# Kernel tuning notes

Hardware: AMD Instinct MI355X
Metric: run time of the kernel (lower is better)

## Reference

```python
import jax, jax.numpy as jnp
import numpy as np

D = 1024      # model dim
H = 16        # heads
DH = D // H   # head dim
T = 1024      # input tokens
B = 2         # batch
P = 4         # persistent tokens
WIN = 256     # sliding window
MH = 4 * D    # neural-memory hidden dim
FF = 4 * D    # ffn hidden dim
EPS = 1e-5


def _layernorm(x, g, b):
    m = jnp.mean(x, axis=-1, keepdims=True)
    v = jnp.mean((x - m) ** 2, axis=-1, keepdims=True)
    return (x - m) * jax.lax.rsqrt(v + EPS) * g + b


def setup_inputs() -> dict:
    key = jax.random.key(0)
    ks = jax.random.split(key, 12)
    s = 0.02
    return {
        "x": jax.random.normal(ks[0], (B, T, D), dtype=jnp.float32),
        "pmem": jax.random.normal(ks[1], (P, D), dtype=jnp.float32) * s,
        # neural memory MLP: dim -> MH -> dim (torch Linear convention W:(out,in))
        "mW1": jax.random.normal(ks[2], (MH, D), dtype=jnp.float32) * s,
        "mb1": jnp.zeros((MH,), dtype=jnp.float32),
        "mW2": jax.random.normal(ks[3], (D, MH), dtype=jnp.float32) * s,
        "mb2": jnp.zeros((D,), dtype=jnp.float32),
        "ln1_g": jnp.ones((D,), dtype=jnp.float32),
        "ln1_b": jnp.zeros((D,), dtype=jnp.float32),
        # MHA packed qkv in-proj and out-proj
        "Wqkv": jax.random.normal(ks[4], (3 * D, D), dtype=jnp.float32) * s,
        "bqkv": jnp.zeros((3 * D,), dtype=jnp.float32),
        "Wo": jax.random.normal(ks[5], (D, D), dtype=jnp.float32) * s,
        "bo": jnp.zeros((D,), dtype=jnp.float32),
        "ln2_g": jnp.ones((D,), dtype=jnp.float32),
        "ln2_b": jnp.zeros((D,), dtype=jnp.float32),
        "fW1": jax.random.normal(ks[6], (FF, D), dtype=jnp.float32) * s,
        "fb1": jnp.zeros((FF,), dtype=jnp.float32),
        "fW2": jax.random.normal(ks[7], (D, FF), dtype=jnp.float32) * s,
        "fb2": jnp.zeros((D,), dtype=jnp.float32),
    }


def _forward(x, pmem, mW1, mb1, mW2, mb2, ln1_g, ln1_b, Wqkv, bqkv, Wo, bo,
             ln2_g, ln2_b, fW1, fb1, fW2, fb2):
    Bc, Tc, Dc = x.shape
    # 1. retrieve from neural long-term memory: 2-layer MLP on x
    mem_ctx = jax.nn.relu(jnp.einsum('btd,hd->bth', x, mW1) + mb1)
    mem_ctx = jnp.einsum('bth,dh->btd', mem_ctx, mW2) + mb2
    # 2. concat persistent tokens, retrieved memory, x along sequence
    pers = jnp.broadcast_to(pmem[None], (Bc, P, Dc))
    aug = jnp.concatenate([pers, mem_ctx, x], axis=1)      # (B, L, D)
    L = aug.shape[1]
    # 3. sliding-window causal attention on norm1(aug)
    h = _layernorm(aug, ln1_g, ln1_b)
    qkv = jnp.einsum('bld,ed->ble', h, Wqkv) + bqkv        # (B, L, 3D)
    q, k, v = jnp.split(qkv, 3, axis=-1)
    q = q.reshape(Bc, L, H, DH)
    k = k.reshape(Bc, L, H, DH)
    v = v.reshape(Bc, L, H, DH)
    scale = 1.0 / np.sqrt(DH).astype(np.float32)
    scores = jnp.einsum('bqhd,bkhd->bhqk', q, k) * scale   # (B, H, L, L)
    i = jnp.arange(L)[:, None]
    j = jnp.arange(L)[None, :]
    allowed = (j <= i) & (j > i - WIN)                     # causal sliding window
    scores = jnp.where(allowed[None, None], scores, jnp.float32(-1e30))
    attn = jax.nn.softmax(scores, axis=-1)
    ctx = jnp.einsum('bhqk,bkhd->bqhd', attn, v).reshape(Bc, L, D)
    h_attn = jnp.einsum('bld,ed->ble', ctx, Wo) + bo
    # 4. residual + FFN
    h_res = aug + h_attn
    f = _layernorm(h_res, ln2_g, ln2_b)
    f = jax.nn.gelu(jnp.einsum('bld,fd->blf', f, fW1) + fb1, approximate=False)
    f = jnp.einsum('blf,df->bld', f, fW2) + fb2
    return h_res + f                                       # (B, P+2T, D)


def reference(x, pmem, mW1, mb1, mW2, mb2, ln1_g, ln1_b, Wqkv, bqkv, Wo, bo,
              ln2_g, ln2_b, fW1, fb1, fW2, fb2):
    return _forward(x, pmem, mW1, mb1, mW2, mb2, ln1_g, ln1_b, Wqkv, bqkv,
                    Wo, bo, ln2_g, ln2_b, fW1, fb1, fW2, fb2)
```

## Files before the change

kernel.cpp:

```cpp
#include <hip/hip_runtime.h>
#include <math.h>

#define D_   1024
#define H_   16
#define DH_  64
#define T_   1024
#define B_   2
#define P_   4
#define L_   2052
#define WIN_ 256
#define MH_  4096
#define FF_  4096

typedef __attribute__((ext_vector_type(8))) short bf16x8;
typedef __attribute__((ext_vector_type(4))) float f32x4;
typedef __attribute__((ext_vector_type(8))) unsigned short ush8;

__device__ __forceinline__ unsigned short f2bf(float f) {
  unsigned int u = __builtin_bit_cast(unsigned int, f);
  u += 0x7fffu + ((u >> 16) & 1u);
  return (unsigned short)(u >> 16);
}
__device__ __forceinline__ float bf2f(unsigned short h) {
  unsigned int u = ((unsigned int)h) << 16;
  return __builtin_bit_cast(float, u);
}

__device__ __forceinline__ void gl16(const unsigned short* g, unsigned short* l) {
  __builtin_amdgcn_global_load_lds(
      (const __attribute__((address_space(1))) unsigned int*)g,
      (__attribute__((address_space(3))) unsigned int*)l, 16, 0, 0);
}

__global__ __launch_bounds__(256)
void cvt7_k(const float* s0, unsigned short* d0, int n0,
            const float* s1, unsigned short* d1, int n1,
            const float* s2, unsigned short* d2, int n2,
            const float* s3, unsigned short* d3, int n3,
            const float* s4, unsigned short* d4, int n4,
            const float* s5, unsigned short* d5, int n5,
            const float* s6, unsigned short* d6, int n6) {
  const float* s; unsigned short* d; int n;
  switch (blockIdx.y) {
    case 0: s = s0; d = d0; n = n0; break;
    case 1: s = s1; d = d1; n = n1; break;
    case 2: s = s2; d = d2; n = n2; break;
    case 3: s = s3; d = d3; n = n3; break;
    case 4: s = s4; d = d4; n = n4; break;
    case 5: s = s5; d = d5; n = n5; break;
    default: s = s6; d = d6; n = n6; break;
  }
  int e = (blockIdx.x * 256 + threadIdx.x) * 4;
  if (e >= n) return;
  float4 v = *(const float4*)(s + e);
  ushort4 o;
  o.x = f2bf(v.x); o.y = f2bf(v.y); o.z = f2bf(v.z); o.w = f2bf(v.w);
  *(ushort4*)(d + e) = o;
}

__global__ __launch_bounds__(256)
void concat_ln1_k(const float* __restrict__ x, const float* __restrict__ pmem,
                  const float* __restrict__ p0, const float* __restrict__ p1,
                  const float* __restrict__ mb2, const float* __restrict__ g,
                  const float* __restrict__ bb,
                  float* __restrict__ aug, unsigned short* __restrict__ hln) {
  const int row = blockIdx.x;
  const int rl  = row % L_;
  const int b   = row / L_;
  const int tid = threadIdx.x;
  const int c   = tid * 4;
  float4 v;
  if (rl < P_) {
    v = *(const float4*)(pmem + rl * D_ + c);
  } else if (rl < P_ + T_) {
    size_t idx = (size_t)(b * T_ + (rl - P_)) * D_ + c;
    float4 a0 = *(const float4*)(p0 + idx);
    float4 a1 = *(const float4*)(p1 + idx);
    float4 bbv = *(const float4*)(mb2 + c);
    v = make_float4(a0.x + a1.x + bbv.x, a0.y + a1.y + bbv.y,
                    a0.z + a1.z + bbv.z, a0.w + a1.w + bbv.w);
  } else {
    v = *(const float4*)(x + (size_t)(b * T_ + (rl - P_ - T_)) * D_ + c);
  }
  *(float4*)(aug + (size_t)row * D_ + c) = v;
  float s  = v.x + v.y + v.z + v.w;
  float sq = v.x * v.x + v.y * v.y + v.z * v.z + v.w * v.w;
  #pragma unroll
  for (int o = 1; o < 64; o <<= 1) { s += __shfl_xor(s, o); sq += __shfl_xor(sq, o); }
  __shared__ float red[8];
  const int wid = tid >> 6;
  if ((tid & 63) == 0) { red[wid] = s; red[4 + wid] = sq; }
  __syncthreads();
  s  = red[0] + red[1] + red[2] + red[3];
  sq = red[4] + red[5] + red[6] + red[7];
  const float mean = s * (1.0f / D_);
  const float var  = sq * (1.0f / D_) - mean * mean;
  const float inv  = rsqrtf(var + 1e-5f);
  float4 gv = *(const float4*)(g + c);
  float4 bv = *(const float4*)(bb + c);
  unsigned short* dst = hln + (size_t)row * D_ + c;
  dst[0] = f2bf((v.x - mean) * inv * gv.x + bv.x);
  dst[1] = f2bf((v.y - mean) * inv * gv.y + bv.y);
  dst[2] = f2bf((v.z - mean) * inv * gv.z + bv.z);
  dst[3] = f2bf((v.w - mean) * inv * gv.w + bv.w);
}

__global__ void reduce10_k(const float* __restrict__ p0, const float* __restrict__ p1,
                           const float* __restrict__ hres, const float* __restrict__ fb2,
                           float* __restrict__ out) {
  int i = blockIdx.x * blockDim.x + threadIdx.x;
  if (i >= (B_ * L_ * D_) / 4) return;
  int e = i * 4;
  int d = e % D_;
  float4 a0 = *(const float4*)(p0 + e);
  float4 a1 = *(const float4*)(p1 + e);
  float4 hr = *(const float4*)(hres + e);
  float4 bb = *(const float4*)(fb2 + d);
  float4 v = make_float4(a0.x + a1.x + hr.x + bb.x, a0.y + a1.y + hr.y + bb.y,
                         a0.z + a1.z + hr.z + bb.z, a0.w + a1.w + hr.w + bb.w);
  *(float4*)(out + e) = v;
}

__global__ __launch_bounds__(256)
void layernorm_k(const float* __restrict__ in, const float* __restrict__ g,
                 const float* __restrict__ bb, unsigned short* __restrict__ out) {
  const int row = blockIdx.x;
  const int tid = threadIdx.x;
  const float* xr = in + (size_t)row * D_;
  float4 v = *(const float4*)(xr + tid * 4);
  float s  = v.x + v.y + v.z + v.w;
  float sq = v.x * v.x + v.y * v.y + v.z * v.z + v.w * v.w;
  #pragma unroll
  for (int o = 1; o < 64; o <<= 1) { s += __shfl_xor(s, o); sq += __shfl_xor(sq, o); }
  __shared__ float red[8];
  const int wid = tid >> 6;
  if ((tid & 63) == 0) { red[wid] = s; red[4 + wid] = sq; }
  __syncthreads();
  s  = red[0] + red[1] + red[2] + red[3];
  sq = red[4] + red[5] + red[6] + red[7];
  const float mean = s * (1.0f / D_);
  const float var  = sq * (1.0f / D_) - mean * mean;
  const float inv  = rsqrtf(var + 1e-5f);
  const int c = tid * 4;
  float4 gv = *(const float4*)(g + c);
  float4 bv = *(const float4*)(bb + c);
  unsigned short* dst = out + (size_t)row * D_ + c;
  dst[0] = f2bf((v.x - mean) * inv * gv.x + bv.x);
  dst[1] = f2bf((v.y - mean) * inv * gv.y + bv.y);
  dst[2] = f2bf((v.z - mean) * inv * gv.z + bv.z);
  dst[3] = f2bf((v.w - mean) * inv * gv.w + bv.w);
}

template<int ACT, int OUTBF, int RESID, int WM, int WN, int NWR, int NWC, int KS, int PART, int SWZ>
__global__ __launch_bounds__(KS * NWR * NWC * 64)
void gemm_bt_k(const unsigned short* __restrict__ A,
               const unsigned short* __restrict__ W,
               const float* __restrict__ bias,
               const float* __restrict__ resid,
               void* __restrict__ Cv,
               int M, int N, int K, int ldK, long long zstride) {
  constexpr int NW = NWR * NWC;
  constexpr int BM = NWR * WM * 16;
  constexpr int BN = NWC * WN * 16;
  constexpr int LPS = BM / (NW * 16) + BN / (NW * 16);
  constexpr int STG = 2 * KS * (BM + BN) * 32 * 2;
  constexpr int RED = (KS > 1) ? BM * BN * 4 : 0;
  constexpr int SBYTES = STG > RED ? STG : RED;
  __shared__ __align__(16) char smem[SBYTES];
  unsigned short* sA = (unsigned short*)smem;
  unsigned short* sB = sA + 2 * KS * BM * 32;

  const int tid  = threadIdx.x;
  const int lane = tid & 63;
  const int wv   = tid >> 6;
  const int grp  = wv / NW;
  const int wg   = wv % NW;
  const int wr   = wg / NWC, wc = wg % NWC;

  int lx = blockIdx.x, ly = blockIdx.y, lz = blockIdx.z;
  if (SWZ) {
    const unsigned int gX = gridDim.x, gY = gridDim.y, gZ = gridDim.z;
    const unsigned int nwg = gX * gY * gZ;
    const unsigned int flat = (blockIdx.z * gY + blockIdx.y) * gX + blockIdx.x;
    const unsigned int q = nwg >> 3;
    const unsigned int g = (flat & 7) * q + (flat >> 3);
    const unsigned int NC = gX * gZ;
    ly = g / NC;
    const unsigned int c = g % NC;
    lx = c / gZ;
    lz = c % gZ;
  }
  const int gm0 = ly * BM;
  const int gn0 = lx * BN;

  const int KperG = K / KS;
  const int NT    = KperG / 32;
  const int zofs  = PART ? lz * K : 0;

  const f32x4 fz = {0.f, 0.f, 0.f, 0.f};
  f32x4 acc[WM][WN];
  #pragma unroll
  for (int i = 0; i < WM; ++i)
    #pragma unroll
    for (int j = 0; j < WN; ++j) acc[i][j] = fz;

  const int srow = lane >> 2;
  const int skq  = (lane & 3) ^ ((lane >> 3) & 3);
  const int skc  = skq * 8;
  const unsigned short* gA = A + (size_t)(gm0 + srow) * ldK + grp * KperG + zofs + skc;
  const unsigned short* gB = W + (size_t)(gn0 + srow) * ldK + grp * KperG + zofs + skc;

  const int fr   = lane & 15;
  const int fkq  = lane >> 4;
  const int fofs = (fr * 4 + (fkq ^ ((fr >> 1) & 3))) * 8;

  auto stage = [&](int d, int k0) {
    unsigned short* dA = sA + (d * KS + grp) * BM * 32;
    unsigned short* dB = sB + (d * KS + grp) * BN * 32;
    #pragma unroll
    for (int t = 0; t < BM / (NW * 16); ++t) {
      const int rr = wg * 16 + t * NW * 16;
      gl16(gA + (size_t)rr * ldK + k0, dA + rr * 32);
    }
    #pragma unroll
    for (int t = 0; t < BN / (NW * 16); ++t) {
      const int rr = wg * 16 + t * NW * 16;
      gl16(gB + (size_t)rr * ldK + k0, dB + rr * 32);
    }
  };

  auto wait_lps = [&]() {
    if constexpr (LPS == 2)      asm volatile("s_waitcnt vmcnt(2)" ::: "memory");
    else if constexpr (LPS == 3) asm volatile("s_waitcnt vmcnt(3)" ::: "memory");
    else if constexpr (LPS == 4) asm volatile("s_waitcnt vmcnt(4)" ::: "memory");
    else                         asm volatile("s_waitcnt vmcnt(0)" ::: "memory");
  };

  stage(0, 0);
  stage(1, 32);
  wait_lps();
  __builtin_amdgcn_s_barrier();
  asm volatile("" ::: "memory");

  for (int kt = 0; kt < NT; ++kt) {
    const int d = kt & 1;
    const unsigned short* lA = sA + (d * KS + grp) * BM * 32;
    const unsigned short* lB = sB + (d * KS + grp) * BN * 32;
    bf16x8 af[WM], bfr[WN];
    #pragma unroll
    for (int i = 0; i < WM; ++i) af[i]  = *(const bf16x8*)&lA[(wr * WM + i) * 512 + fofs];
    #pragma unroll
    for (int j = 0; j < WN; ++j) bfr[j] = *(const bf16x8*)&lB[(wc * WN + j) * 512 + fofs];
    asm volatile("s_waitcnt lgkmcnt(0)" ::: "memory");
    __builtin_amdgcn_s_barrier();
    asm volatile("" ::: "memory");
    if (kt + 2 < NT) stage(d, (kt + 2) * 32);
    __builtin_amdgcn_s_setprio(1);
    #pragma unroll
    for (int i = 0; i < WM; ++i)
      #pragma unroll
      for (int j = 0; j < WN; ++j)
        acc[i][j] = __builtin_amdgcn_mfma_f32_16x16x32_bf16(af[i], bfr[j], acc[i][j], 0, 0, 0);
    __builtin_amdgcn_s_setprio(0);
    if (kt + 1 < NT) {
      if (kt + 2 < NT) wait_lps();
      else asm volatile("s_waitcnt vmcnt(0)" ::: "memory");
      __builtin_amdgcn_s_barrier();
      asm volatile("" ::: "memory");
    }
  }

  if (KS > 1) {
    __syncthreads();
    f32x4* sR = (f32x4*)smem;
    const int tg = tid & (NW * 64 - 1);
    for (int g = 1; g < KS; ++g) {
      if (grp == g) {
        #pragma unroll
        for (int i = 0; i < WM; ++i)
          #pragma unroll
          for (int j = 0; j < WN; ++j) sR[(tg * WM + i) * WN + j] = acc[i][j];
      }
      __syncthreads();
      if (grp == 0) {
        #pragma unroll
        for (int i = 0; i < WM; ++i)
          #pragma unroll
          for (int j = 0; j < WN; ++j) {
            f32x4 t = sR[(tg * WM + i) * WN + j];
            #pragma unroll
            for (int r = 0; r < 4; ++r) acc[i][j][r] += t[r];
          }
      }
      __syncthreads();
    }
    if (grp != 0) return;
  }

  const int rq = (lane >> 4) * 4;
  if (PART) {
    float* Pout = (float*)Cv + (size_t)lz * zstride;
    #pragma unroll
    for (int i = 0; i < WM; ++i) {
      #pragma unroll
      for (int j = 0; j < WN; ++j) {
        const int col = gn0 + wc * WN * 16 + j * 16 + fr;
        #pragma unroll
        for (int r = 0; r < 4; ++r) {
          const int row = gm0 + wr * WM * 16 + i * 16 + rq + r;
          if (row < M) Pout[(size_t)row * N + col] = acc[i][j][r];
        }
      }
    }
    return;
  }
  #pragma unroll
  for (int i = 0; i < WM; ++i) {
    #pragma unroll
    for (int j = 0; j < WN; ++j) {
      const int col = gn0 + wc * WN * 16 + j * 16 + fr;
      const float bcol = bias[col];
      #pragma unroll
      for (int r = 0; r < 4; ++r) {
        const int row = gm0 + wr * WM * 16 + i * 16 + rq + r;
        if (row < M) {
          float v = acc[i][j][r] + bcol;
          if (RESID) v += resid[(size_t)row * N + col];
          if (ACT == 1) v = fmaxf(v, 0.f);
          if (ACT == 2) {
            float t = 0.7978845608f * v * (1.0f + 0.044715f * v * v);
            float e = __expf(2.0f * t);
            v = v - __fdividef(v, e + 1.0f);
          }
          if (OUTBF) ((unsigned short*)Cv)[(size_t)row * N + col] = f2bf(v);
          else       ((float*)Cv)[(size_t)row * N + col] = v;
        }
      }
    }
  }
}

__global__ __launch_bounds__(256)
void attn_k(const unsigned short* __restrict__ qkv, unsigned short* __restrict__ ctx) {
  __shared__ unsigned short Kb[64][72];
  __shared__ unsigned short Vt[64][72];
  __shared__ unsigned short Ps[4][16][72];
  const int tid  = threadIdx.x;
  const int lane = tid & 63;
  const int w    = tid >> 6;
  const int l15  = lane & 15;
  const int l4   = lane >> 4;
  const int qb   = blockIdx.x * 64;
  const int h    = blockIdx.y;
  const int b    = blockIdx.z;

  int qrow = qb + w * 16 + l15;
  if (qrow >= L_) qrow = L_ - 1;
  const unsigned short* qp = qkv + ((size_t)(b * L_ + qrow)) * 3072 + h * 64;
  bf16x8 aq0, aq1;
  #pragma unroll
  for (int e = 0; e < 8; ++e) {
    aq0[e] = (short)f2bf(bf2f(qp[l4 * 8 + e]) * 0.125f);
    aq1[e] = (short)f2bf(bf2f(qp[32 + l4 * 8 + e]) * 0.125f);
  }

  const f32x4 fz = {0.f, 0.f, 0.f, 0.f};
  f32x4 acc_o[4];
  #pragma unroll
  for (int j = 0; j < 4; ++j) acc_o[j] = fz;
  float m_[4], ls[4];
  #pragma unroll
  for (int r = 0; r < 4; ++r) { m_[r] = -3.0e38f; ls[r] = 0.f; }

  int k0 = qb - WIN_;
  if (k0 < 0) k0 = 0;

  for (int kb = k0; kb <= qb; kb += 64) {
    #pragma unroll
    for (int c = tid; c < 512; c += 256) {
      const int row = c >> 3;
      const int cc  = (c & 7) * 8;
      const int g   = kb + row;
      ush8 kv8 = {0, 0, 0, 0, 0, 0, 0, 0}, vv8 = kv8;
      if (g < L_) {
        const unsigned short* base = qkv + ((size_t)(b * L_ + g)) * 3072 + h * 64 + cc;
        kv8 = *(const ush8*)(base + 1024);
        vv8 = *(const ush8*)(base + 2048);
      }
      *(ush8*)&Kb[row][cc] = kv8;
      #pragma unroll
      for (int e = 0; e < 8; ++e) Vt[cc + e][row] = vv8[e];
    }
    __syncthreads();

    f32x4 s[4];
    #pragma unroll
    for (int kt = 0; kt < 4; ++kt) {
      bf16x8 bk0 = *(const bf16x8*)&Kb[kt * 16 + l15][l4 * 8];
      bf16x8 bk1 = *(const bf16x8*)&Kb[kt * 16 + l15][32 + l4 * 8];
      f32x4 t = __builtin_amdgcn_mfma_f32_16x16x32_bf16(aq0, bk0, fz, 0, 0, 0);
      s[kt]   = __builtin_amdgcn_mfma_f32_16x16x32_bf16(aq1, bk1, t,  0, 0, 0);
    }

    #pragma unroll
    for (int r = 0; r < 4; ++r) {
      const int qg = qb + w * 16 + l4 * 4 + r;
      float rm = -3.0e38f;
      #pragma unroll
      for (int kt = 0; kt < 4; ++kt) {
        const int kg = kb + kt * 16 + l15;
        const bool ok = (kg <= qg) && (kg + WIN_ > qg);
        rm = fmaxf(rm, ok ? s[kt][r] : -3.0e38f);
      }
      rm = fmaxf(rm, __shfl_xor(rm, 1));
      rm = fmaxf(rm, __shfl_xor(rm, 2));
      rm = fmaxf(rm, __shfl_xor(rm, 4));
      rm = fmaxf(rm, __shfl_xor(rm, 8));
      const float mn = fmaxf(m_[r], rm);
      const float sf = __expf(m_[r] - mn);
      m_[r] = mn;
      float ps = 0.f;
      #pragma unroll
      for (int kt = 0; kt < 4; ++kt) {
        const int kg = kb + kt * 16 + l15;
        const bool ok = (kg <= qg) && (kg + WIN_ > qg);
        const float p = ok ? __expf(s[kt][r] - mn) : 0.f;
        ps += p;
        Ps[w][l4 * 4 + r][kt * 16 + l15] = f2bf(p);
      }
      ps += __shfl_xor(ps, 1);
      ps += __shfl_xor(ps, 2);
      ps += __shfl_xor(ps, 4);
      ps += __shfl_xor(ps, 8);
      ls[r] = ls[r] * sf + ps;
      #pragma unroll
      for (int j = 0; j < 4; ++j) acc_o[j][r] *= sf;
    }

    #pragma unroll
    for (int ks = 0; ks < 2; ++ks) {
      bf16x8 pa = *(const bf16x8*)&Ps[w][l15][ks * 32 + l4 * 8];
      #pragma unroll
      for (int j = 0; j < 4; ++j) {
        bf16x8 vb = *(const bf16x8*)&Vt[j * 16 + l15][ks * 32 + l4 * 8];
        acc_o[j] = __builtin_amdgcn_mfma_f32_16x16x32_bf16(pa, vb, acc_o[j], 0, 0, 0);
      }
    }
    __syncthreads();
  }

  #pragma unroll
  for (int r = 0; r < 4; ++r) {
    const int qg = qb + w * 16 + l4 * 4 + r;
    if (qg < L_) {
      const float inv = 1.0f / ls[r];
      unsigned short* dst = ctx + ((size_t)(b * L_ + qg)) * 1024 + h * 64 + l15;
      #pragma unroll
      for (int j = 0; j < 4; ++j) dst[j * 16] = f2bf(acc_o[j][r] * inv);
    }
  }
}

extern "C" void kernel_launch(void* const* d_in, const int* in_sizes, int n_in,
                              void* d_out, int out_size, void* d_ws, size_t ws_size,
                              hipStream_t stream) {
  (void)in_sizes; (void)n_in; (void)out_size; (void)ws_size;
  const float* x    = (const float*)d_in[0];
  const float* pmem = (const float*)d_in[1];
  const float* mW1  = (const float*)d_in[2];
  const float* mb1  = (const float*)d_in[3];
  const float* mW2  = (const float*)d_in[4];
  const float* mb2  = (const float*)d_in[5];
  const float* ln1g = (const float*)d_in[6];
  const float* ln1b = (const float*)d_in[7];
  const float* Wqkv = (const float*)d_in[8];
  const float* bqkv = (const float*)d_in[9];
  const float* Wo   = (const float*)d_in[10];
  const float* bo   = (const float*)d_in[11];
  const float* ln2g = (const float*)d_in[12];
  const float* ln2b = (const float*)d_in[13];
  const float* fW1  = (const float*)d_in[14];
  const float* fb1  = (const float*)d_in[15];
  const float* fW2  = (const float*)d_in[16];
  const float* fb2  = (const float*)d_in[17];
  float* outp = (float*)d_out;
  char* ws = (char*)d_ws;

  unsigned short* w1b   = (unsigned short*)(ws + 0ull);
  unsigned short* w2b   = (unsigned short*)(ws + 8388608ull);
  unsigned short* wqkvb = (unsigned short*)(ws + 16777216ull);
  unsigned short* wob   = (unsigned short*)(ws + 23068672ull);
  unsigned short* fw1b  = (unsigned short*)(ws + 25165824ull);
  unsigned short* fw2b  = (unsigned short*)(ws + 33554432ull);
  const size_t S = 41943040ull;
  float* aug  = (float*)(ws + S);
  float* hres = (float*)(ws + S + 16809984ull);
  unsigned short* hlnbuf = (unsigned short*)(ws + S + 33619968ull);
  char* R = ws + S + 42270720ull;
  unsigned short* xb   = (unsigned short*)(R);
  unsigned short* h1   = (unsigned short*)(R + 4194304ull);
  unsigned short* qkvb = (unsigned short*)(R);
  unsigned short* f1   = (unsigned short*)(R + 15826944ull);
  unsigned short* hln  = hlnbuf;
  unsigned short* ctxb = hlnbuf;
  unsigned short* hln2 = hlnbuf;
  float* g2p = hres;
  float* g10p = aug;
  const long long Z10 = 8404992LL;

  const int BT = B_ * T_;
  const int BL = B_ * L_;
  const int NE4 = B_ * L_ * D_ / 4;

  cvt7_k<<<dim3((MH_ * D_ / 4 + 255) / 256, 7), 256, 0, stream>>>(
      x, xb, B_ * T_ * D_,  mW1, w1b, MH_ * D_,  mW2, w2b, D_ * MH_,
      Wqkv, wqkvb, 3 * D_ * D_,  Wo, wob, D_ * D_,
      fW1, fw1b, FF_ * D_,  fW2, fw2b, D_ * FF_);

  gemm_bt_k<1, 1, 0, 4, 4, 2, 4, 1, 0, 0><<<dim3(MH_ / 256, BT / 128), 512, 0, stream>>>(xb, w1b, mb1, nullptr, h1, BT, MH_, D_, D_, 0);
  gemm_bt_k<0, 0, 0, 4, 4, 2, 2, 1, 1, 1><<<dim3(D_ / 128, BT / 128, 2), 256, 0, stream>>>(h1, w2b, nullptr, nullptr, g2p, BT, D_, MH_ / 2, MH_, (long long)BT * D_);
  concat_ln1_k<<<dim3(BL), 256, 0, stream>>>(x, pmem, g2p, g2p + (size_t)BT * D_, mb2, ln1g, ln1b, aug, hln);
  gemm_bt_k<0, 1, 0, 4, 4, 2, 4, 1, 0, 0><<<dim3(3 * D_ / 256, (BL + 127) / 128), 512, 0, stream>>>(hln, wqkvb, bqkv, nullptr, qkvb, BL, 3 * D_, D_, D_, 0);
  attn_k<<<dim3((L_ + 63) / 64, H_, B_), 256, 0, stream>>>(qkvb, ctxb);
  gemm_bt_k<0, 0, 1, 2, 4, 4, 1, 1, 0, 0><<<dim3(D_ / 64, (BL + 127) / 128), 256, 0, stream>>>(ctxb, wob, bo, aug, hres, BL, D_, D_, D_, 0);
  layernorm_k<<<dim3(BL), 256, 0, stream>>>(hres, ln2g, ln2b, hln2);
  gemm_bt_k<2, 1, 0, 4, 4, 2, 4, 1, 0, 0><<<dim3(FF_ / 256, (BL + 127) / 128), 512, 0, stream>>>(hln2, fw1b, fb1, nullptr, f1, BL, FF_, D_, D_, 0);
  gemm_bt_k<0, 0, 0, 4, 4, 2, 4, 1, 1, 0><<<dim3(D_ / 256, (BL + 127) / 128, 2), 512, 0, stream>>>(f1, fw2b, nullptr, nullptr, g10p, BL, D_, FF_ / 2, FF_, Z10);
  reduce10_k<<<dim3((NE4 + 255) / 256), 256, 0, stream>>>(g10p, g10p + Z10, hres, fb2, outp);
}
```

Measured before the change: 339.8 us.

## Split-K four ways with bf16 partials and widen attention query tile

The two down-projection GEMMs now split K into four partitions instead of two. The FFN down-projection partials are stored as bf16 to halve the partial-sum traffic, and the reduction kernels sum four partials. The attention kernel processes 128 query rows per block with 512 threads, so each K/V tile load is shared by more queries. The cost is a coarser attention grid, extra rounding error from the bf16 partials, and more partial buffers and reduction reads.

```diff
diff --git a/kernel.cpp b/kernel.cpp
--- a/kernel.cpp
+++ b/kernel.cpp
@@ -61,6 +61,7 @@
 __global__ __launch_bounds__(256)
 void concat_ln1_k(const float* __restrict__ x, const float* __restrict__ pmem,
                   const float* __restrict__ p0, const float* __restrict__ p1,
+                  const float* __restrict__ p2, const float* __restrict__ p3,
                   const float* __restrict__ mb2, const float* __restrict__ g,
                   const float* __restrict__ bb,
                   float* __restrict__ aug, unsigned short* __restrict__ hln) {
@@ -76,9 +77,13 @@
     size_t idx = (size_t)(b * T_ + (rl - P_)) * D_ + c;
     float4 a0 = *(const float4*)(p0 + idx);
     float4 a1 = *(const float4*)(p1 + idx);
+    float4 a2 = *(const float4*)(p2 + idx);
+    float4 a3 = *(const float4*)(p3 + idx);
     float4 bbv = *(const float4*)(mb2 + c);
-    v = make_float4(a0.x + a1.x + bbv.x, a0.y + a1.y + bbv.y,
-                    a0.z + a1.z + bbv.z, a0.w + a1.w + bbv.w);
+    v = make_float4(a0.x + a1.x + a2.x + a3.x + bbv.x,
+                    a0.y + a1.y + a2.y + a3.y + bbv.y,
+                    a0.z + a1.z + a2.z + a3.z + bbv.z,
+                    a0.w + a1.w + a2.w + a3.w + bbv.w);
   } else {
     v = *(const float4*)(x + (size_t)(b * T_ + (rl - P_ - T_)) * D_ + c);
   }
@@ -105,19 +110,27 @@
   dst[3] = f2bf((v.w - mean) * inv * gv.w + bv.w);
 }
 
-__global__ void reduce10_k(const float* __restrict__ p0, const float* __restrict__ p1,
+__global__ void reduce10_k(const unsigned short* __restrict__ q0,
+                           const unsigned short* __restrict__ q1,
+                           const unsigned short* __restrict__ q2,
+                           const unsigned short* __restrict__ q3,
                            const float* __restrict__ hres, const float* __restrict__ fb2,
                            float* __restrict__ out) {
   int i = blockIdx.x * blockDim.x + threadIdx.x;
   if (i >= (B_ * L_ * D_) / 4) return;
   int e = i * 4;
   int d = e % D_;
-  float4 a0 = *(const float4*)(p0 + e);
-  float4 a1 = *(const float4*)(p1 + e);
+  ushort4 u0 = *(const ushort4*)(q0 + e);
+  ushort4 u1 = *(const ushort4*)(q1 + e);
+  ushort4 u2 = *(const ushort4*)(q2 + e);
+  ushort4 u3 = *(const ushort4*)(q3 + e);
   float4 hr = *(const float4*)(hres + e);
   float4 bb = *(const float4*)(fb2 + d);
-  float4 v = make_float4(a0.x + a1.x + hr.x + bb.x, a0.y + a1.y + hr.y + bb.y,
-                         a0.z + a1.z + hr.z + bb.z, a0.w + a1.w + hr.w + bb.w);
+  float4 v;
+  v.x = bf2f(u0.x) + bf2f(u1.x) + bf2f(u2.x) + bf2f(u3.x) + hr.x + bb.x;
+  v.y = bf2f(u0.y) + bf2f(u1.y) + bf2f(u2.y) + bf2f(u3.y) + hr.y + bb.y;
+  v.z = bf2f(u0.z) + bf2f(u1.z) + bf2f(u2.z) + bf2f(u3.z) + hr.z + bb.z;
+  v.w = bf2f(u0.w) + bf2f(u1.w) + bf2f(u2.w) + bf2f(u3.w) + hr.w + bb.w;
   *(float4*)(out + e) = v;
 }
 
@@ -158,7 +171,7 @@
                const float* __restrict__ bias,
                const float* __restrict__ resid,
                void* __restrict__ Cv,
-               int M, int N, int K, int ldK, long long zstride) {
+               int M, int N, int K, int ldK, long long zs1, long long zs2) {
   constexpr int NW = NWR * NWC;
   constexpr int BM = NWR * WM * 16;
   constexpr int BN = NWC * WN * 16;
@@ -299,7 +312,7 @@
 
   const int rq = (lane >> 4) * 4;
   if (PART) {
-    float* Pout = (float*)Cv + (size_t)lz * zstride;
+    char* Pb = (char*)Cv + (size_t)(lz & 1) * zs1 + (size_t)(lz >> 1) * zs2;
     #pragma unroll
     for (int i = 0; i < WM; ++i) {
       #pragma unroll
@@ -308,7 +321,10 @@
         #pragma unroll
         for (int r = 0; r < 4; ++r) {
           const int row = gm0 + wr * WM * 16 + i * 16 + rq + r;
-          if (row < M) Pout[(size_t)row * N + col] = acc[i][j][r];
+          if (row < M) {
+            if (OUTBF) ((unsigned short*)Pb)[(size_t)row * N + col] = f2bf(acc[i][j][r]);
+            else       ((float*)Pb)[(size_t)row * N + col] = acc[i][j][r];
+          }
         }
       }
     }
@@ -340,17 +356,17 @@
   }
 }
 
-__global__ __launch_bounds__(256)
+__global__ __launch_bounds__(512)
 void attn_k(const unsigned short* __restrict__ qkv, unsigned short* __restrict__ ctx) {
   __shared__ unsigned short Kb[64][72];
   __shared__ unsigned short Vt[64][72];
-  __shared__ unsigned short Ps[4][16][72];
+  __shared__ unsigned short Ps[8][16][72];
   const int tid  = threadIdx.x;
   const int lane = tid & 63;
   const int w    = tid >> 6;
   const int l15  = lane & 15;
   const int l4   = lane >> 4;
-  const int qb   = blockIdx.x * 64;
+  const int qb   = blockIdx.x * 128;
   const int h    = blockIdx.y;
   const int b    = blockIdx.z;
 
@@ -375,9 +391,9 @@
   int k0 = qb - WIN_;
   if (k0 < 0) k0 = 0;
 
-  for (int kb = k0; kb <= qb; kb += 64) {
-    #pragma unroll
-    for (int c = tid; c < 512; c += 256) {
+  for (int kb = k0; kb <= qb + 64; kb += 64) {
+    {
+      const int c   = tid;
       const int row = c >> 3;
       const int cc  = (c & 7) * 8;
       const int g   = kb + row;
@@ -505,8 +521,10 @@
   unsigned short* ctxb = hlnbuf;
   unsigned short* hln2 = hlnbuf;
   float* g2p = hres;
-  float* g10p = aug;
-  const long long Z10 = 8404992LL;
+  const long long G2S  = 8404992LL;
+  const long long G2S2 = 46432256LL;
+  const long long Z10a = 8404992LL;
+  const long long Z10b = 33619968LL;
 
   const int BT = B_ * T_;
   const int BL = B_ * L_;
@@ -517,14 +535,21 @@
       Wqkv, wqkvb, 3 * D_ * D_,  Wo, wob, D_ * D_,
       fW1, fw1b, FF_ * D_,  fW2, fw2b, D_ * FF_);
 
-  gemm_bt_k<1, 1, 0, 4, 4, 2, 4, 1, 0, 0><<<dim3(MH_ / 256, BT / 128), 512, 0, stream>>>(xb, w1b, mb1, nullptr, h1, BT, MH_, D_, D_, 0);
-  gemm_bt_k<0, 0, 0, 4, 4, 2, 2, 1, 1, 1><<<dim3(D_ / 128, BT / 128, 2), 256, 0, stream>>>(h1, w2b, nullptr, nullptr, g2p, BT, D_, MH_ / 2, MH_, (long long)BT * D_);
-  concat_ln1_k<<<dim3(BL), 256, 0, stream>>>(x, pmem, g2p, g2p + (size_t)BT * D_, mb2, ln1g, ln1b, aug, hln);
-  gemm_bt_k<0, 1, 0, 4, 4, 2, 4, 1, 0, 0><<<dim3(3 * D_ / 256, (BL + 127) / 128), 512, 0, stream>>>(hln, wqkvb, bqkv, nullptr, qkvb, BL, 3 * D_, D_, D_, 0);
-  attn_k<<<dim3((L_ + 63) / 64, H_, B_), 256, 0, stream>>>(qkvb, ctxb);
-  gemm_bt_k<0, 0, 1, 2, 4, 4, 1, 1, 0, 0><<<dim3(D_ / 64, (BL + 127) / 128), 256, 0, stream>>>(ctxb, wob, bo, aug, hres, BL, D_, D_, D_, 0);
+  gemm_bt_k<1, 1, 0, 4, 4, 2, 4, 1, 0, 0><<<dim3(MH_ / 256, BT / 128), 512, 0, stream>>>(xb, w1b, mb1, nullptr, h1, BT, MH_, D_, D_, 0, 0);
+  gemm_bt_k<0, 0, 0, 4, 4, 2, 2, 1, 1, 1><<<dim3(D_ / 128, BT / 128, 4), 256, 0, stream>>>(h1, w2b, nullptr, nullptr, g2p, BT, D_, MH_ / 4, MH_, G2S, G2S2);
+  concat_ln1_k<<<dim3(BL), 256, 0, stream>>>(x, pmem,
+      g2p, (float*)((char*)g2p + G2S), (float*)((char*)g2p + G2S2), (float*)((char*)g2p + G2S + G2S2),
+      mb2, ln1g, ln1b, aug, hln);
+  gemm_bt_k<0, 1, 0, 4, 4, 2, 4, 1, 0, 0><<<dim3(3 * D_ / 256, (BL + 127) / 128), 512, 0, stream>>>(hln, wqkvb, bqkv, nullptr, qkvb, BL, 3 * D_, D_, D_, 0, 0);
+  attn_k<<<dim3((L_ + 127) / 128, H_, B_), 512, 0, stream>>>(qkvb, ctxb);
+  gemm_bt_k<0, 0, 1, 2, 4, 4, 1, 1, 0, 0><<<dim3(D_ / 64, (BL + 127) / 128), 256, 0, stream>>>(ctxb, wob, bo, aug, hres, BL, D_, D_, D_, 0, 0);
   layernorm_k<<<dim3(BL), 256, 0, stream>>>(hres, ln2g, ln2b, hln2);
-  gemm_bt_k<2, 1, 0, 4, 4, 2, 4, 1, 0, 0><<<dim3(FF_ / 256, (BL + 127) / 128), 512, 0, stream>>>(hln2, fw1b, fb1, nullptr, f1, BL, FF_, D_, D_, 0);
-  gemm_bt_k<0, 0, 0, 4, 4, 2, 4, 1, 1, 0><<<dim3(D_ / 256, (BL + 127) / 128, 2), 512, 0, stream>>>(f1, fw2b, nullptr, nullptr, g10p, BL, D_, FF_ / 2, FF_, Z10);
-  reduce10_k<<<dim3((NE4 + 255) / 256), 256, 0, stream>>>(g10p, g10p + Z10, hres, fb2, outp);
-}
+  gemm_bt_k<2, 1, 0, 4, 4, 2, 4, 1, 0, 0><<<dim3(FF_ / 256, (BL + 127) / 128), 512, 0, stream>>>(hln2, fw1b, fb1, nullptr, f1, BL, FF_, D_, D_, 0, 0);
+  gemm_bt_k<0, 1, 0, 4, 4, 2, 4, 1, 1, 0><<<dim3(D_ / 256, (BL + 127) / 128, 4), 512, 0, stream>>>(f1, fw2b, nullptr, nullptr, (void*)aug, BL, D_, FF_ / 4, FF_, Z10a, Z10b);
+  reduce10_k<<<dim3((NE4 + 255) / 256), 256, 0, stream>>>(
+      (const unsigned short*)aug,
+      (const unsigned short*)((char*)aug + Z10a),
+      (const unsigned short*)((char*)aug + Z10b),
+      (const unsigned short*)((char*)aug + Z10a + Z10b),
+      hres, fb2, outp);
+}
```

After: 332.4 us, median of 2. 1.02x faster.
